# Performance work log

Measured on AMD Instinct MI355X. Metric: run time of the kernel, lower is better.

Reference implementation:

```python
import jax, jax.numpy as jnp
import numpy as np

B, T, E = 2, 2048, 1024
H = 16
D = E // H  # head_dim = 64


def setup_inputs() -> dict:
    key = jax.random.key(0)
    ks = jax.random.split(key, 9)
    s = 1.0 / np.sqrt(E)
    inp = {"x": jax.random.normal(ks[0], (B, T, E), dtype=jnp.float32)}
    # Linear params (torch nn.Linear: y = x @ W.T + b)
    inp["Wq"] = jax.random.uniform(ks[1], (E, E), jnp.float32, -s, s)
    inp["bq"] = jax.random.uniform(ks[2], (E,), jnp.float32, -s, s)
    inp["Wk"] = jax.random.uniform(ks[3], (E, E), jnp.float32, -s, s)
    inp["bk"] = jax.random.uniform(ks[4], (E,), jnp.float32, -s, s)
    inp["Wv"] = jax.random.uniform(ks[5], (E, E), jnp.float32, -s, s)
    inp["bv"] = jax.random.uniform(ks[6], (E,), jnp.float32, -s, s)
    inp["Wo"] = jax.random.uniform(ks[7], (E, E), jnp.float32, -s, s)
    inp["bo"] = jax.random.uniform(ks[8], (E,), jnp.float32, -s, s)
    return inp


def reference(x, Wq, bq, Wk, bk, Wv, bv, Wo, bo):
    # QKV projections, reshape to [B, H, T, D]
    def split_heads(y):
        return y.reshape(B, T, H, D).transpose(0, 2, 1, 3)

    Q = split_heads(x @ Wq.T + bq)
    K = split_heads(x @ Wk.T + bk)
    V = split_heads(x @ Wv.T + bv)

    scale = 1.0 / jnp.sqrt(jnp.asarray(D, x.dtype))
    scores = jnp.einsum("bhqd,bhkd->bhqk", Q, K) * scale  # [B,H,T,T]
    attn = jax.nn.softmax(scores, axis=-1)
    out = jnp.einsum("bhqk,bhkd->bhqd", attn, V)  # [B,H,T,D]
    out = out.transpose(0, 2, 1, 3).reshape(B, T, E)
    # dropout is identity in eval mode
    return out @ Wo.T + bo
```

## Files before the change

### kernel.cpp

```cpp
#include <hip/hip_runtime.h>
#include <math.h>

#define BB 2
#define TT 2048
#define EE 1024
#define HH 16
#define DD 64
#define MM (BB*TT)
#define KK EE

typedef short bf16x8 __attribute__((ext_vector_type(8)));
typedef float f32x4  __attribute__((ext_vector_type(4)));

__device__ __forceinline__ unsigned short f2bf(float f) {
  unsigned int u = __float_as_uint(f);
  u = (u + 0x7FFFu + ((u >> 16) & 1u)) >> 16;
  return (unsigned short)u;
}

__device__ __forceinline__ void async16(const void* g, void* l) {
  __builtin_amdgcn_global_load_lds(
      (const __attribute__((address_space(1))) unsigned int*)g,
      (__attribute__((address_space(3))) unsigned int*)l, 16, 0, 0);
}

__global__ __launch_bounds__(256) void to_bf16(
    const float* __restrict__ x,  const float* __restrict__ wq,
    const float* __restrict__ wk, const float* __restrict__ wv,
    const float* __restrict__ wo,
    unsigned short* __restrict__ xh, unsigned short* __restrict__ wcat,
    unsigned short* __restrict__ woh)
{
  int c = blockIdx.x * 256 + threadIdx.x;
  const float* src; unsigned short* dst; int off;
  if (c < 1048576) { src = x; dst = xh; off = c; }
  else {
    int r = c - 1048576;
    int w = r >> 18;
    off = r & 262143;
    if      (w == 0) { src = wq; dst = wcat; }
    else if (w == 1) { src = wk; dst = wcat + (1 << 20); }
    else if (w == 2) { src = wv; dst = wcat + (2 << 20); }
    else             { src = wo; dst = woh; }
  }
  float4 v = ((const float4*)src)[off];
  ushort4 h;
  h.x = f2bf(v.x); h.y = f2bf(v.y); h.z = f2bf(v.z); h.w = f2bf(v.w);
  ((ushort4*)dst)[off] = h;
}

template<int MODE>
__global__ __launch_bounds__(512) void gemm_bf16(
    const unsigned short* __restrict__ A, const unsigned short* __restrict__ B,
    const float* __restrict__ b0p, const float* __restrict__ b1p,
    const float* __restrict__ b2p,
    unsigned short* __restrict__ oq, unsigned short* __restrict__ ok,
    unsigned short* __restrict__ ov, float* __restrict__ ofp, float qscale)
{
  constexpr int NT = (MODE == 0) ? 128 : 64;
  constexpr int JN = NT / 32;
  constexpr int BROWS = NT * 32;
  constexpr int TOT = (MODE == 0) ? 16 : 12;
  __shared__ unsigned short S[(MODE == 0) ? 17408 : 12288];

  const int tid  = threadIdx.x;
  const int lane = tid & 63;
  const int wv   = tid >> 6;
  const int col  = lane & 15;
  const int quad = lane >> 4;
  const int wm = (wv & 3) * 32;
  const int wn = (wv >> 2) * (NT / 2);
  const int m0 = blockIdx.x * 128;
  const int n0 = blockIdx.y * NT;

  const int srow = lane >> 2;
  const int sw16 = (((lane & 3) ^ ((lane >> 2) & 3)) << 3);
  const int fswA = ((quad ^ (col & 3)) << 3);

  auto stage = [&](int kt, int b) {
#pragma unroll
    for (int s = 0; s < 2; ++s) {
      const int t = wv * 2 + s;
      if (t < TOT) {
        const unsigned short* src; int rb, g0, loff;
        if (t < 8) { src = A; rb = t * 16;       g0 = m0; loff = b * 4096; }
        else       { src = B; rb = (t - 8) * 16; g0 = n0; loff = 8192 + b * BROWS; }
        async16(src + (size_t)(g0 + rb + srow) * KK + kt + sw16,
                S + loff + rb * 32);
      }
    }
  };

  f32x4 acc[2][JN];
  const f32x4 z = {0.f, 0.f, 0.f, 0.f};
#pragma unroll
  for (int i = 0; i < 2; ++i)
#pragma unroll
    for (int j = 0; j < JN; ++j) acc[i][j] = z;

  stage(0, 0);
  __syncthreads();

  for (int kt = 0; kt < KK; kt += 32) {
    const int buf = (kt >> 5) & 1;
    if (kt + 32 < KK) stage(kt + 32, buf ^ 1);

    const unsigned short* Asb = S + buf * 4096;
    const unsigned short* Bsb = S + 8192 + buf * BROWS;
    bf16x8 bf[JN];
#pragma unroll
    for (int j = 0; j < JN; ++j)
      bf[j] = *(const bf16x8*)(Bsb + (wn + j * 16 + col) * 32 + fswA);
#pragma unroll
    for (int i = 0; i < 2; ++i) {
      bf16x8 af = *(const bf16x8*)(Asb + (wm + i * 16 + col) * 32 + fswA);
#pragma unroll
      for (int j = 0; j < JN; ++j)
        acc[i][j] = __builtin_amdgcn_mfma_f32_16x16x32_bf16(af, bf[j], acc[i][j], 0, 0, 0);
    }
    __syncthreads();
  }

  unsigned short* Cs = S;
  if (MODE == 0) {
    const int region = n0 >> 10;
    const float* bias = (region == 0) ? b0p : (region == 1) ? b1p : b2p;
    const float scl = (region == 0) ? qscale : 1.0f;
    const int nlbase = n0 & 1023;
    const int h0 = nlbase >> 6;
    const int b = m0 >> 11, t0 = m0 & (TT - 1);
    if (region < 2) {
#pragma unroll
      for (int i = 0; i < 2; ++i)
#pragma unroll
        for (int j = 0; j < 4; ++j) {
          const int nt = wn + j * 16 + col;
          const float bs = bias[nlbase + nt];
#pragma unroll
          for (int r = 0; r < 4; ++r) {
            const int mt = wm + i * 16 + quad * 4 + r;
            Cs[mt * 136 + nt] = f2bf((acc[i][j][r] + bs) * scl);
          }
        }
      __syncthreads();
      unsigned short* dst = (region == 0) ? oq : ok;
#pragma unroll
      for (int s = 0; s < 4; ++s) {
        const int u = s * 512 + tid;
        const int mt = u >> 4, hs = (u >> 3) & 1, ch = u & 7;
        const size_t g = ((size_t)(b * HH + h0 + hs) * TT + t0 + mt) * DD + ch * 8;
        *(uint4*)(dst + g) = *(const uint4*)(Cs + mt * 136 + hs * 64 + ch * 8);
      }
    } else {
#pragma unroll
      for (int i = 0; i < 2; ++i)
#pragma unroll
        for (int j = 0; j < 4; ++j) {
          const int nt = wn + j * 16 + col;
          const float bs = bias[nlbase + nt];
          ushort4 pk;
          pk.x = f2bf(acc[i][j][0] + bs);
          pk.y = f2bf(acc[i][j][1] + bs);
          pk.z = f2bf(acc[i][j][2] + bs);
          pk.w = f2bf(acc[i][j][3] + bs);
          *(ushort4*)(Cs + nt * 136 + wm + i * 16 + quad * 4) = pk;
        }
      __syncthreads();
#pragma unroll
      for (int s = 0; s < 4; ++s) {
        const int u = s * 512 + tid;
        const int nt = u >> 4, ch = u & 15;
        const int d = nt & 63, hs = nt >> 6;
        const size_t g = ((size_t)(b * HH + h0 + hs) * DD + d) * TT + t0 + ch * 8;
        *(uint4*)(ov + g) = *(const uint4*)(Cs + nt * 136 + ch * 8);
      }
    }
  } else {
#pragma unroll
    for (int i = 0; i < 2; ++i) {
#pragma unroll
      for (int j = 0; j < JN; ++j) {
        const int n = n0 + wn + j * 16 + col;
        const float bs = b0p[n];
#pragma unroll
        for (int r = 0; r < 4; ++r) {
          const int m = m0 + wm + i * 16 + quad * 4 + r;
          ofp[(size_t)m * EE + n] = acc[i][j][r] + bs;
        }
      }
    }
  }
}

__global__ __launch_bounds__(512) void flash_mfma(
    const unsigned short* __restrict__ Qb, const unsigned short* __restrict__ Kb,
    const unsigned short* __restrict__ Vtb, unsigned short* __restrict__ ctx)
{
  __shared__ unsigned short QPs[128 * 72];
  __shared__ unsigned short Ks[2][64 * 64];
  __shared__ unsigned short Vts[2][64 * 64];

  const int tid  = threadIdx.x;
  const int lane = tid & 63;
  const int wv   = tid >> 6;
  const int col  = lane & 15;
  const int quad = lane >> 4;
  const int wm   = wv * 16;
  const int gid  = blockIdx.x;
  const int bh   = gid & 31;
  const int q0   = (gid >> 5) * 128;

  const unsigned short* Qg = Qb  + (size_t)bh * TT * DD;
  const unsigned short* Kg = Kb  + (size_t)bh * TT * DD;
  const unsigned short* Vg = Vtb + (size_t)bh * DD * TT;

  const int srow = lane >> 3;
  const int sw16 = (((lane & 7) ^ ((lane >> 3) & 7)) << 3);
  const int cxor = (col & 7);

  auto stage_kv = [&](int kt, int b) {
#pragma unroll
    for (int s = 0; s < 2; ++s) {
      const int rb = (wv & 3) * 16 + s * 8;
      if (wv < 4)
        async16(Kg + (size_t)(kt + rb + srow) * DD + sw16, &Ks[b][rb * 64]);
      else
        async16(Vg + (size_t)(rb + srow) * TT + kt + sw16, &Vts[b][rb * 64]);
    }
  };

#pragma unroll
  for (int s = 0; s < 2; ++s) {
    const int rb = wv * 16 + s * 8;
    async16(Qg + (size_t)(q0 + rb + srow) * DD + sw16, &QPs[rb * 64]);
  }
  stage_kv(0, 0);
  __syncthreads();

  bf16x8 aq[2];
#pragma unroll
  for (int h = 0; h < 2; ++h)
    aq[h] = *(const bf16x8*)(QPs + (wm + col) * 64 +
                             (((h * 4 + quad) ^ cxor) << 3));
  __syncthreads();

  f32x4 o_acc[4];
  float lpart = 0.f;
  const f32x4 z = {0.f, 0.f, 0.f, 0.f};
#pragma unroll
  for (int j = 0; j < 4; ++j) o_acc[j] = z;

  for (int kt = 0; kt < TT; kt += 64) {
    const int buf = (kt >> 6) & 1;
    if (kt + 64 < TT) stage_kv(kt + 64, buf ^ 1);

    f32x4 sacc[4];
#pragma unroll
    for (int j = 0; j < 4; ++j) sacc[j] = z;

#pragma unroll
    for (int j = 0; j < 4; ++j) {
      bf16x8 bk0 = *(const bf16x8*)(Ks[buf] + (j * 16 + col) * 64 + ((quad ^ cxor) << 3));
      bf16x8 bk1 = *(const bf16x8*)(Ks[buf] + (j * 16 + col) * 64 + (((4 + quad) ^ cxor) << 3));
      sacc[j] = __builtin_amdgcn_mfma_f32_16x16x32_bf16(bk0, aq[0], sacc[j], 0, 0, 0);
      sacc[j] = __builtin_amdgcn_mfma_f32_16x16x32_bf16(bk1, aq[1], sacc[j], 0, 0, 0);
    }

    {
      const int prow = (wm + col) * 72;
      float lp = 0.f;
#pragma unroll
      for (int j = 0; j < 4; ++j) {
        float p0 = __builtin_amdgcn_exp2f(sacc[j][0]);
        float p1 = __builtin_amdgcn_exp2f(sacc[j][1]);
        float p2 = __builtin_amdgcn_exp2f(sacc[j][2]);
        float p3 = __builtin_amdgcn_exp2f(sacc[j][3]);
        lp += (p0 + p1) + (p2 + p3);
        uint2 w;
        w.x = __builtin_amdgcn_perm(__float_as_uint(p1), __float_as_uint(p0), 0x07060302u);
        w.y = __builtin_amdgcn_perm(__float_as_uint(p3), __float_as_uint(p2), 0x07060302u);
        *(uint2*)(QPs + prow + j * 16 + quad * 4) = w;
      }
      lpart += lp;
    }

    bf16x8 ap0 = *(const bf16x8*)(QPs + (wm + col) * 72 + quad * 8);
    bf16x8 ap1 = *(const bf16x8*)(QPs + (wm + col) * 72 + 32 + quad * 8);

#pragma unroll
    for (int j = 0; j < 4; ++j) {
      bf16x8 bv0 = *(const bf16x8*)(Vts[buf] + (j * 16 + col) * 64 + ((quad ^ cxor) << 3));
      bf16x8 bv1 = *(const bf16x8*)(Vts[buf] + (j * 16 + col) * 64 + (((4 + quad) ^ cxor) << 3));
      o_acc[j] = __builtin_amdgcn_mfma_f32_16x16x32_bf16(ap0, bv0, o_acc[j], 0, 0, 0);
      o_acc[j] = __builtin_amdgcn_mfma_f32_16x16x32_bf16(ap1, bv1, o_acc[j], 0, 0, 0);
    }

    __syncthreads();
  }

  unsigned short* Cs = &Ks[0][0];
  const int b = bh >> 4, h = bh & 15;
  float l = lpart;
  l += __shfl_xor(l, 16);
  l += __shfl_xor(l, 32);
#pragma unroll
  for (int r = 0; r < 4; ++r) {
    const float inv = 1.0f / __shfl(l, quad * 4 + r);
    const int trow = wm + quad * 4 + r;
#pragma unroll
    for (int j = 0; j < 4; ++j) {
      const int n = j * 16 + col;
      const int ch = ((n >> 3) ^ (trow & 7)) << 3;
      Cs[trow * 64 + ch + (n & 7)] = f2bf(o_acc[j][r] * inv);
    }
  }
  __syncthreads();
#pragma unroll
  for (int s = 0; s < 2; ++s) {
    const int u = s * 512 + tid;
    const int mr = u >> 3, ch = u & 7;
    const size_t g = ((size_t)(b * TT + q0 + mr)) * EE + h * DD + ch * 8;
    const int chs = (ch ^ (mr & 7)) << 3;
    *(uint4*)(ctx + g) = *(const uint4*)(Cs + mr * 64 + chs);
  }
}

extern "C" void kernel_launch(void* const* d_in, const int* in_sizes, int n_in,
                              void* d_out, int out_size, void* d_ws, size_t ws_size,
                              hipStream_t stream) {
  const float* x  = (const float*)d_in[0];
  const float* Wq = (const float*)d_in[1];
  const float* bq = (const float*)d_in[2];
  const float* Wk = (const float*)d_in[3];
  const float* bk = (const float*)d_in[4];
  const float* Wv = (const float*)d_in[5];
  const float* bv = (const float*)d_in[6];
  const float* Wo = (const float*)d_in[7];
  const float* bo = (const float*)d_in[8];

  unsigned short* p = (unsigned short*)d_ws;
  const size_t XN = (size_t)MM * EE;
  const size_t WN = (size_t)EE * EE;
  unsigned short* x_h    = p;           p += XN;
  unsigned short* Wcat_h = p;           p += 3 * WN;
  unsigned short* Wo_h   = p;           p += WN;
  unsigned short* Qb     = p;           p += XN;
  unsigned short* Kb     = p;           p += XN;
  unsigned short* Vtb    = p;           p += XN;
  unsigned short* ctx_h  = x_h;

  to_bf16<<<8192, 256, 0, stream>>>(x, Wq, Wk, Wv, Wo, x_h, Wcat_h, Wo_h);

  const float qscale = 0.125f * 1.44269504088896f;

  gemm_bf16<0><<<dim3(MM / 128, 3 * EE / 128), 512, 0, stream>>>(
      x_h, Wcat_h, bq, bk, bv, Qb, Kb, Vtb, nullptr, qscale);

  flash_mfma<<<dim3((TT / 128) * BB * HH), 512, 0, stream>>>(Qb, Kb, Vtb, ctx_h);

  gemm_bf16<2><<<dim3(MM / 128, EE / 64), 512, 0, stream>>>(
      ctx_h, Wo_h, bo, nullptr, nullptr,
      nullptr, nullptr, nullptr, (float*)d_out, 1.0f);
}
```

Baseline: 189.7 us.

## Restructure flash attention with 32x32 MFMA, key-split waves and software-pipelined QK

Rewrites the attention kernel to use 32x32x16 bf16 MFMAs, with waves split across query rows and two key halves. P stays in registers through cvt_pk and permlane32 swaps instead of round-tripping through LDS. K/V staging grows to a 4-slot ring with two tiles in flight. The next tile's QK product is computed while the current tile's PV runs, with priority hints, and the two key-half partial outputs are reduced in LDS at the end. The aim is to cut LDS traffic and barrier stalls and overlap softmax with MFMA work, at the cost of more registers and a more complex epilogue.

```diff
diff --git a/kernel.cpp b/kernel.cpp
--- a/kernel.cpp
+++ b/kernel.cpp
@@ -11,11 +11,23 @@
 
 typedef short bf16x8 __attribute__((ext_vector_type(8)));
 typedef float f32x4  __attribute__((ext_vector_type(4)));
+typedef float f32x16 __attribute__((ext_vector_type(16)));
+typedef unsigned int u32x4 __attribute__((ext_vector_type(4)));
 
 __device__ __forceinline__ unsigned short f2bf(float f) {
   unsigned int u = __float_as_uint(f);
   u = (u + 0x7FFFu + ((u >> 16) & 1u)) >> 16;
   return (unsigned short)u;
+}
+
+__device__ __forceinline__ unsigned int cvtpk(float lo, float hi) {
+  unsigned int r;
+  asm("v_cvt_pk_bf16_f32 %0, %1, %2" : "=v"(r) : "v"(lo), "v"(hi));
+  return r;
+}
+
+__device__ __forceinline__ void plswap(unsigned int &a, unsigned int &b) {
+  asm("v_permlane32_swap_b32 %0, %1" : "+v"(a), "+v"(b));
 }
 
 __device__ __forceinline__ void async16(const void* g, void* l) {
@@ -192,20 +204,21 @@
   }
 }
 
-__global__ __launch_bounds__(512) void flash_mfma(
+__global__ __launch_bounds__(512, 4) void flash_mfma(
     const unsigned short* __restrict__ Qb, const unsigned short* __restrict__ Kb,
     const unsigned short* __restrict__ Vtb, unsigned short* __restrict__ ctx)
 {
-  __shared__ unsigned short QPs[128 * 72];
-  __shared__ unsigned short Ks[2][64 * 64];
-  __shared__ unsigned short Vts[2][64 * 64];
+  __shared__ unsigned short Qs[128 * 64];
+  __shared__ unsigned short Ks[4][64 * 64];
+  __shared__ unsigned short Vts[4][64 * 64];
 
   const int tid  = threadIdx.x;
   const int lane = tid & 63;
   const int wv   = tid >> 6;
-  const int col  = lane & 15;
-  const int quad = lane >> 4;
-  const int wm   = wv * 16;
+  const int lq   = lane & 31;
+  const int hf   = lane >> 5;
+  const int wq   = wv & 3;
+  const int wk2  = wv >> 2;
   const int gid  = blockIdx.x;
   const int bh   = gid & 31;
   const int q0   = (gid >> 5) * 128;
@@ -216,110 +229,184 @@
 
   const int srow = lane >> 3;
   const int sw16 = (((lane & 7) ^ ((lane >> 3) & 7)) << 3);
-  const int cxor = (col & 7);
-
-  auto stage_kv = [&](int kt, int b) {
-#pragma unroll
-    for (int s = 0; s < 2; ++s) {
-      const int rb = (wv & 3) * 16 + s * 8;
-      if (wv < 4)
-        async16(Kg + (size_t)(kt + rb + srow) * DD + sw16, &Ks[b][rb * 64]);
-      else
-        async16(Vg + (size_t)(rb + srow) * TT + kt + sw16, &Vts[b][rb * 64]);
-    }
+
+  const int rbK = wq * 16;
+  const bool isK = (wv < 4);
+  const unsigned short* g0 =
+      (isK ? Kg + (size_t)(rbK + srow) * DD : Vg + (size_t)(rbK + srow) * TT) + sw16;
+  const unsigned short* g1 = g0 + (isK ? 8 * DD : 8 * TT);
+  unsigned short* l0 = (isK ? &Ks[0][0] : &Vts[0][0]) + rbK * 64;
+  unsigned short* l1 = l0 + 8 * 64;
+  const int gstep = isK ? 64 * DD : 64;
+
+  auto stage_kv = [&](int ti, int slot) {
+    const size_t go = (size_t)ti * gstep;
+    async16(g0 + go, l0 + slot * 4096);
+    async16(g1 + go, l1 + slot * 4096);
   };
+
+  int koff[4], voff[2][2];
+#pragma unroll
+  for (int s = 0; s < 4; ++s)
+    koff[s] = ((wk2 * 32 + lq) * 64 + (((2 * s + hf) ^ (lane & 7)) << 3)) * 2;
+#pragma unroll
+  for (int m = 0; m < 2; ++m)
+#pragma unroll
+    for (int sg = 0; sg < 2; ++sg)
+      voff[m][sg] = ((m * 32 + lq) * 64 +
+                     (((wk2 * 4 + 2 * sg + hf) ^ (lane & 7)) << 3)) * 2;
 
 #pragma unroll
   for (int s = 0; s < 2; ++s) {
     const int rb = wv * 16 + s * 8;
-    async16(Qg + (size_t)(q0 + rb + srow) * DD + sw16, &QPs[rb * 64]);
+    async16(Qg + (size_t)(q0 + rb + srow) * DD + sw16, &Qs[rb * 64]);
   }
   stage_kv(0, 0);
+  stage_kv(1, 1);
   __syncthreads();
 
-  bf16x8 aq[2];
-#pragma unroll
-  for (int h = 0; h < 2; ++h)
-    aq[h] = *(const bf16x8*)(QPs + (wm + col) * 64 +
-                             (((h * 4 + quad) ^ cxor) << 3));
+  bf16x8 aq[4];
+#pragma unroll
+  for (int s = 0; s < 4; ++s)
+    aq[s] = *(const bf16x8*)(Qs + (wq * 32 + lq) * 64 +
+                             (((2 * s + hf) ^ (lane & 7)) << 3));
+
+  const f32x16 z16 = {0.f,0.f,0.f,0.f,0.f,0.f,0.f,0.f,
+                      0.f,0.f,0.f,0.f,0.f,0.f,0.f,0.f};
+  f32x16 o_acc[2], sacc, nsacc;
+  o_acc[0] = z16; o_acc[1] = z16;
+  float lpart = 0.f;
+
+  {
+    const char* Kp = (const char*)&Ks[0][0];
+    sacc = z16;
+#pragma unroll
+    for (int s = 0; s < 4; ++s) {
+      bf16x8 ak = *(const bf16x8*)(Kp + koff[s]);
+      sacc = __builtin_amdgcn_mfma_f32_32x32x16_bf16(ak, aq[s], sacc, 0, 0, 0);
+    }
+  }
+
+#define BODY(T, S0, S1, S2, DOSTAGE, DOQK, VMC, SIN, SOUT) do {               \
+    if (DOSTAGE) stage_kv((T) + 2, S2);                                       \
+    asm volatile("s_waitcnt vmcnt(" #VMC ")" ::: "memory");                   \
+    __builtin_amdgcn_sched_barrier(0);                                        \
+    __builtin_amdgcn_s_barrier();                                             \
+    __builtin_amdgcn_sched_barrier(0);                                        \
+    bf16x8 pa0, pa1;                                                          \
+    {      \
+      float e0 = __builtin_amdgcn_exp2f(SIN[0]);                              \
+      float e1 = __builtin_amdgcn_exp2f(SIN[1]);                              \
+      float e2 = __builtin_amdgcn_exp2f(SIN[2]);                              \
+      float e3 = __builtin_amdgcn_exp2f(SIN[3]);                              \
+      float e4 = __builtin_amdgcn_exp2f(SIN[4]);                              \
+      float e5 = __builtin_amdgcn_exp2f(SIN[5]);                              \
+      float e6 = __builtin_amdgcn_exp2f(SIN[6]);                              \
+      float e7 = __builtin_amdgcn_exp2f(SIN[7]);                              \
+      lpart += ((e0 + e1) + (e2 + e3)) + ((e4 + e5) + (e6 + e7));             \
+      unsigned int a0 = cvtpk(e0, e1), b0 = cvtpk(e4, e5);                    \
+      unsigned int a1 = cvtpk(e2, e3), b1 = cvtpk(e6, e7);                    \
+      plswap(a0, b0); plswap(a1, b1);                                         \
+      u32x4 w = {a0, a1, b0, b1};                                             \
+      pa0 = __builtin_bit_cast(bf16x8, w);                                    \
+    }                                                                         \
+    {                                                     \
+      float e0 = __builtin_amdgcn_exp2f(SIN[8]);                              \
+      float e1 = __builtin_amdgcn_exp2f(SIN[9]);                              \
+      float e2 = __builtin_amdgcn_exp2f(SIN[10]);                             \
+      float e3 = __builtin_amdgcn_exp2f(SIN[11]);                             \
+      float e4 = __builtin_amdgcn_exp2f(SIN[12]);                             \
+      float e5 = __builtin_amdgcn_exp2f(SIN[13]);                             \
+      float e6 = __builtin_amdgcn_exp2f(SIN[14]);                             \
+      float e7 = __builtin_amdgcn_exp2f(SIN[15]);                             \
+      lpart += ((e0 + e1) + (e2 + e3)) + ((e4 + e5) + (e6 + e7));             \
+      unsigned int a0 = cvtpk(e0, e1), b0 = cvtpk(e4, e5);                    \
+      unsigned int a1 = cvtpk(e2, e3), b1 = cvtpk(e6, e7);                    \
+      plswap(a0, b0); plswap(a1, b1);                                         \
+      u32x4 w = {a0, a1, b0, b1};                                             \
+      pa1 = __builtin_bit_cast(bf16x8, w);                                    \
+    }                                                                         \
+    __builtin_amdgcn_s_setprio(1);                                            \
+    if (DOQK) {                      \
+      const char* Kp = (const char*)&Ks[S1][0];                               \
+      f32x16 ns = z16;                                                        \
+      _Pragma("unroll")                                                       \
+      for (int s = 0; s < 4; ++s) {                                           \
+        bf16x8 ak = *(const bf16x8*)(Kp + koff[s]);                           \
+        ns = __builtin_amdgcn_mfma_f32_32x32x16_bf16(ak, aq[s], ns, 0, 0, 0); \
+      }                                                                       \
+      SOUT = ns;                                                              \
+    }                                                                         \
+    {                                                              \
+      const char* Vp = (const char*)&Vts[S0][0];                              \
+      _Pragma("unroll")                                                       \
+      for (int m = 0; m < 2; ++m) {                                           \
+        bf16x8 v0 = *(const bf16x8*)(Vp + voff[m][0]);                        \
+        bf16x8 v1 = *(const bf16x8*)(Vp + voff[m][1]);                        \
+        o_acc[m] = __builtin_amdgcn_mfma_f32_32x32x16_bf16(pa0, v0, o_acc[m], 0, 0, 0); \
+        o_acc[m] = __builtin_amdgcn_mfma_f32_32x32x16_bf16(pa1, v1, o_acc[m], 0, 0, 0); \
+      }                                                                       \
+    }                                                                         \
+    __builtin_amdgcn_s_setprio(0);                                            \
+  } while (0)
+
+  for (int t = 0; t < 28; t += 4) {
+    BODY(t + 0, 0, 1, 2, 1, 1, 2, sacc, nsacc);
+    BODY(t + 1, 1, 2, 3, 1, 1, 2, nsacc, sacc);
+    BODY(t + 2, 2, 3, 0, 1, 1, 2, sacc, nsacc);
+    BODY(t + 3, 3, 0, 1, 1, 1, 2, nsacc, sacc);
+  }
+  BODY(28, 0, 1, 2, 1, 1, 2, sacc, nsacc);
+  BODY(29, 1, 2, 3, 1, 1, 2, nsacc, sacc);
+  BODY(30, 2, 3, 0, 0, 1, 0, sacc, nsacc);
+  BODY(31, 3, 0, 1, 0, 0, 0, nsacc, sacc);
+#undef BODY
+
+  float* Qf = (float*)&Qs[0];
+  float* Of = (float*)&Ks[0][0];
+  unsigned short* Cs = &Vts[0][0];
+  const int bq = bh >> 4, head = bh & 15;
+
+  float lw = lpart + __shfl_xor(lpart, 32);
+  if (lane < 32) Qf[wv * 32 + lane] = lw;
   __syncthreads();
 
-  f32x4 o_acc[4];
-  float lpart = 0.f;
-  const f32x4 z = {0.f, 0.f, 0.f, 0.f};
-#pragma unroll
-  for (int j = 0; j < 4; ++j) o_acc[j] = z;
-
-  for (int kt = 0; kt < TT; kt += 64) {
-    const int buf = (kt >> 6) & 1;
-    if (kt + 64 < TT) stage_kv(kt + 64, buf ^ 1);
-
-    f32x4 sacc[4];
-#pragma unroll
-    for (int j = 0; j < 4; ++j) sacc[j] = z;
-
-#pragma unroll
-    for (int j = 0; j < 4; ++j) {
-      bf16x8 bk0 = *(const bf16x8*)(Ks[buf] + (j * 16 + col) * 64 + ((quad ^ cxor) << 3));
-      bf16x8 bk1 = *(const bf16x8*)(Ks[buf] + (j * 16 + col) * 64 + (((4 + quad) ^ cxor) << 3));
-      sacc[j] = __builtin_amdgcn_mfma_f32_16x16x32_bf16(bk0, aq[0], sacc[j], 0, 0, 0);
-      sacc[j] = __builtin_amdgcn_mfma_f32_16x16x32_bf16(bk1, aq[1], sacc[j], 0, 0, 0);
-    }
-
-    {
-      const int prow = (wm + col) * 72;
-      float lp = 0.f;
-#pragma unroll
-      for (int j = 0; j < 4; ++j) {
-        float p0 = __builtin_amdgcn_exp2f(sacc[j][0]);
-        float p1 = __builtin_amdgcn_exp2f(sacc[j][1]);
-        float p2 = __builtin_amdgcn_exp2f(sacc[j][2]);
-        float p3 = __builtin_amdgcn_exp2f(sacc[j][3]);
-        lp += (p0 + p1) + (p2 + p3);
-        uint2 w;
-        w.x = __builtin_amdgcn_perm(__float_as_uint(p1), __float_as_uint(p0), 0x07060302u);
-        w.y = __builtin_amdgcn_perm(__float_as_uint(p3), __float_as_uint(p2), 0x07060302u);
-        *(uint2*)(QPs + prow + j * 16 + quad * 4) = w;
-      }
-      lpart += lp;
-    }
-
-    bf16x8 ap0 = *(const bf16x8*)(QPs + (wm + col) * 72 + quad * 8);
-    bf16x8 ap1 = *(const bf16x8*)(QPs + (wm + col) * 72 + 32 + quad * 8);
-
-#pragma unroll
-    for (int j = 0; j < 4; ++j) {
-      bf16x8 bv0 = *(const bf16x8*)(Vts[buf] + (j * 16 + col) * 64 + ((quad ^ cxor) << 3));
-      bf16x8 bv1 = *(const bf16x8*)(Vts[buf] + (j * 16 + col) * 64 + (((4 + quad) ^ cxor) << 3));
-      o_acc[j] = __builtin_amdgcn_mfma_f32_16x16x32_bf16(ap0, bv0, o_acc[j], 0, 0, 0);
-      o_acc[j] = __builtin_amdgcn_mfma_f32_16x16x32_bf16(ap1, bv1, o_acc[j], 0, 0, 0);
-    }
-
-    __syncthreads();
-  }
-
-  unsigned short* Cs = &Ks[0][0];
-  const int b = bh >> 4, h = bh & 15;
-  float l = lpart;
-  l += __shfl_xor(l, 16);
-  l += __shfl_xor(l, 32);
-#pragma unroll
-  for (int r = 0; r < 4; ++r) {
-    const float inv = 1.0f / __shfl(l, quad * 4 + r);
-    const int trow = wm + quad * 4 + r;
-#pragma unroll
-    for (int j = 0; j < 4; ++j) {
-      const int n = j * 16 + col;
-      const int ch = ((n >> 3) ^ (trow & 7)) << 3;
-      Cs[trow * 64 + ch + (n & 7)] = f2bf(o_acc[j][r] * inv);
-    }
+  if (wv >= 4) {
+#pragma unroll
+    for (int m = 0; m < 2; ++m)
+#pragma unroll
+      for (int r = 0; r < 16; ++r) {
+        const int ql = (r & 3) + 8 * (r >> 2) + 4 * hf;
+        Of[wq * 2048 + ql * 64 + m * 32 + lq] = o_acc[m][r];
+      }
   }
   __syncthreads();
+
+  if (wv < 4) {
+    float linv[16];
+#pragma unroll
+    for (int r = 0; r < 16; ++r) {
+      const int ql = (r & 3) + 8 * (r >> 2) + 4 * hf;
+      linv[r] = 1.0f / (Qf[wv * 32 + ql] + Qf[(wv + 4) * 32 + ql]);
+    }
+#pragma unroll
+    for (int m = 0; m < 2; ++m)
+#pragma unroll
+      for (int r = 0; r < 16; ++r) {
+        const int ql = (r & 3) + 8 * (r >> 2) + 4 * hf;
+        const float val =
+            (o_acc[m][r] + Of[wq * 2048 + ql * 64 + m * 32 + lq]) * linv[r];
+        const int row = wq * 32 + ql, d = m * 32 + lq;
+        Cs[row * 64 + (((d >> 3) ^ (row & 7)) << 3) + (d & 7)] = f2bf(val);
+      }
+  }
+  __syncthreads();
+
 #pragma unroll
   for (int s = 0; s < 2; ++s) {
     const int u = s * 512 + tid;
     const int mr = u >> 3, ch = u & 7;
-    const size_t g = ((size_t)(b * TT + q0 + mr)) * EE + h * DD + ch * 8;
+    const size_t g = ((size_t)(bq * TT + q0 + mr)) * EE + head * DD + ch * 8;
     const int chs = (ch ^ (mr & 7)) << 3;
     *(uint4*)(ctx + g) = *(const uint4*)(Cs + mr * 64 + chs);
   }
```

Measured after the change: 192.1 us. About the same (+1.3%).
